# Kernel tuning notes

Measured on AMD Instinct MI355X. Metric: run time of the kernel, lower is better.

## Reference

```python
import jax, jax.numpy as jnp
import numpy as np

N_NODES = 100000
N_EDGES = 1600000
IN_DIM = 128
HID_DIM = 256
OUT_DIM = 128
K = 10
ALPHA = 0.1


def setup_inputs() -> dict:
    key = jax.random.key(0)
    k1, k2, k3, k4, k5, k6, k7 = jax.random.split(key, 7)
    feat = jax.random.normal(k1, (N_NODES, IN_DIM), dtype=jnp.float32)
    src = jax.random.randint(k2, (N_EDGES,), 0, N_NODES, dtype=jnp.int64)
    dst = jax.random.randint(k3, (N_EDGES,), 0, N_NODES, dtype=jnp.int64)
    # MLP params (Linear: y = x @ W + b), kaiming-ish scale
    W1 = jax.random.normal(k4, (IN_DIM, HID_DIM), dtype=jnp.float32) * (1.0 / np.sqrt(IN_DIM))
    b1 = jax.random.normal(k5, (HID_DIM,), dtype=jnp.float32) * 0.01
    W2 = jax.random.normal(k6, (HID_DIM, OUT_DIM), dtype=jnp.float32) * (1.0 / np.sqrt(HID_DIM))
    b2 = jax.random.normal(k7, (OUT_DIM,), dtype=jnp.float32) * 0.01
    return {"feat": feat, "W1": W1, "b1": b1, "W2": W2, "b2": b2, "src": src, "dst": dst}


def reference(feat, W1, b1, W2, b2, src, dst):
    N = feat.shape[0]
    # dgl.add_self_loop: append (i, i) for every node
    loops = jnp.arange(N, dtype=src.dtype)
    src_sl = jnp.concatenate([src, loops])
    dst_sl = jnp.concatenate([dst, loops])
    # symmetric normalization from in-degrees (with self-loops), clamped >= 1
    deg = jax.ops.segment_sum(jnp.ones_like(dst_sl, dtype=feat.dtype), dst_sl, num_segments=N)
    norm = jnp.clip(deg, 1.0) ** -0.5  # [N]

    # APPNP propagation: h <- (1-alpha) * D^-1/2 A D^-1/2 h + alpha * feat
    def hop(h, _):
        m = (h * norm[:, None])[src_sl]                      # gather scaled src feats [E+N, D]
        agg = jax.ops.segment_sum(m, dst_sl, num_segments=N)  # scatter-sum to dst [N, D]
        h = (1.0 - ALPHA) * (agg * norm[:, None]) + ALPHA * feat
        return h, None

    h, _ = jax.lax.scan(hop, feat, None, length=K)
    # 2-layer MLP: Linear -> ReLU -> Linear
    x = jax.nn.relu(h @ W1 + b1)
    return x @ W2 + b2
```

## Files before the change

kernel.cpp:

```cpp
#include <hip/hip_runtime.h>

#define IN_DIM 128
#define HID_DIM 256
#define OUT_DIM 128
#define KHOPS 10

#define NBUCK 32
#define NBLK_B 640

typedef __attribute__((ext_vector_type(8))) short bf16x8;
typedef __attribute__((ext_vector_type(4))) float f32x4;

__device__ __forceinline__ unsigned short f2bf(float x) {
    unsigned int b = __float_as_uint(x);
    unsigned int r = (b + 0x7FFFu + ((b >> 16) & 1u)) >> 16;
    return (unsigned short)r;
}
__device__ __forceinline__ unsigned int pack_bf2(float lo, float hi) {
    return (unsigned int)f2bf(lo) | ((unsigned int)f2bf(hi) << 16);
}
__device__ __forceinline__ float bf_lo(unsigned int u) { return __uint_as_float(u << 16); }
__device__ __forceinline__ float bf_hi(unsigned int u) { return __uint_as_float(u & 0xFFFF0000u); }


__global__ void count_init(int* __restrict__ cnt, int* __restrict__ fill,
                           int* __restrict__ bucket_cnt, int N) {
    int i = blockIdx.x * blockDim.x + threadIdx.x;
    if (i < N) { cnt[i] = 0; fill[i] = 0; }
    if (i < NBUCK) bucket_cnt[i] = 0;
}

__global__ __launch_bounds__(256) void bucket_count(
    const int* __restrict__ dst, int* __restrict__ bucket_cnt,
    int* __restrict__ blk_base, int E) {
    __shared__ int h[NBUCK];
    int tid = threadIdx.x;
    if (tid < NBUCK) h[tid] = 0;
    __syncthreads();
    for (int e = blockIdx.x * 256 + tid; e < E; e += NBLK_B * 256)
        atomicAdd(&h[dst[e] >> 12], 1);
    __syncthreads();
    if (tid < NBUCK)
        blk_base[blockIdx.x * NBUCK + tid] = atomicAdd(&bucket_cnt[tid], h[tid]);
}

__global__ void bucket_scan(const int* __restrict__ bucket_cnt,
                            int* __restrict__ bucket_start) {
    __shared__ int s[NBUCK];
    int tid = threadIdx.x;
    int v = bucket_cnt[tid];
    s[tid] = v;
    __syncthreads();
    for (int off = 1; off < NBUCK; off <<= 1) {
        int t = (tid >= off) ? s[tid - off] : 0;
        __syncthreads();
        s[tid] += t;
        __syncthreads();
    }
    bucket_start[tid] = s[tid] - v;
}

__global__ __launch_bounds__(256) void bucket_fill(
    const int* __restrict__ src, const int* __restrict__ dst,
    const int* __restrict__ bucket_start, const int* __restrict__ blk_base,
    uint2* __restrict__ pairs, int E) {
    __shared__ int base[NBUCK];
    int tid = threadIdx.x;
    if (tid < NBUCK) base[tid] = bucket_start[tid] + blk_base[blockIdx.x * NBUCK + tid];
    __syncthreads();
    for (int e = blockIdx.x * 256 + tid; e < E; e += NBLK_B * 256) {
        int d = dst[e], s = src[e];
        int p = atomicAdd(&base[d >> 12], 1);
        pairs[p] = make_uint2((unsigned)s, (unsigned)d);
    }
}

__global__ void count_pairs(const uint2* __restrict__ pairs, int* __restrict__ cnt, int E) {
    int e = blockIdx.x * blockDim.x + threadIdx.x;
    if (e < E) atomicAdd(&cnt[pairs[e].y], 1);
}

__global__ void norm_kernel(const int* __restrict__ cnt, float* __restrict__ norm, int N) {
    int i = blockIdx.x * blockDim.x + threadIdx.x;
    if (i < N) {
        float deg = (float)(cnt[i] + 1);
        norm[i] = rsqrtf(deg);
    }
}

__global__ void scan_block(const int* __restrict__ cnt, int* __restrict__ row_ptr,
                           int* __restrict__ bsum, int N) {
    __shared__ int s[256];
    int tid = threadIdx.x;
    int gid = blockIdx.x * 256 + tid;
    int v = (gid < N) ? cnt[gid] : 0;
    s[tid] = v;
    __syncthreads();
    for (int off = 1; off < 256; off <<= 1) {
        int t = (tid >= off) ? s[tid - off] : 0;
        __syncthreads();
        s[tid] += t;
        __syncthreads();
    }
    if (gid < N) row_ptr[gid] = s[tid] - v;
    if (tid == 255) bsum[blockIdx.x] = s[255];
}

__global__ void scan_top(int* __restrict__ bsum, int nb) {
    __shared__ int s[512];
    int tid = threadIdx.x;
    int v = (tid < nb) ? bsum[tid] : 0;
    s[tid] = v;
    __syncthreads();
    for (int off = 1; off < 512; off <<= 1) {
        int t = (tid >= off) ? s[tid - off] : 0;
        __syncthreads();
        s[tid] += t;
        __syncthreads();
    }
    if (tid < nb) bsum[tid] = s[tid] - v;
}

__global__ void scan_add(int* __restrict__ row_ptr, const int* __restrict__ bsum,
                         int N, int E) {
    int gid = blockIdx.x * 256 + threadIdx.x;
    if (gid < N) row_ptr[gid] += bsum[blockIdx.x];
    if (gid == 0) row_ptr[N] = E;
}

__global__ void fill_pairs(const uint2* __restrict__ pairs, const int* __restrict__ row_ptr,
                           int* __restrict__ fill, int* __restrict__ col, int E) {
    int e = blockIdx.x * blockDim.x + threadIdx.x;
    if (e < E) {
        uint2 pr = pairs[e];
        int p = atomicAdd(&fill[pr.y], 1);
        col[row_ptr[pr.y] + p] = (int)pr.x;
    }
}


__global__ void pack_w1(const float* __restrict__ W1, short* __restrict__ W1s) {
    int i = blockIdx.x * 256 + threadIdx.x;
    if (i >= 16 * 4 * 64 * 8) return;
    int j = i & 7, l = (i >> 3) & 63, kf = (i >> 9) & 3, rf = i >> 11;
    int k = kf * 32 + (l >> 4) * 8 + j;
    int r = rf * 16 + (l & 15);
    W1s[i] = (short)f2bf(W1[(size_t)k * HID_DIM + r]);
}

__global__ void pack_w2(const float* __restrict__ W2, short* __restrict__ W2s) {
    int i = blockIdx.x * 256 + threadIdx.x;
    if (i >= 8 * 8 * 64 * 8) return;
    int j = i & 7, l = (i >> 3) & 63, kf = (i >> 9) & 7, rf = i >> 12;
    int k = kf * 32 + (l >> 4) * 8 + j;
    int r = rf * 16 + (l & 15);
    W2s[i] = (short)f2bf(W2[(size_t)k * OUT_DIM + r]);
}


__global__ void init_g(const float* __restrict__ feat, const float* __restrict__ norm,
                       unsigned int* __restrict__ sh, unsigned int* __restrict__ ffeat,
                       int N) {
    int idx = blockIdx.x * blockDim.x + threadIdx.x;
    int total = N * 64;
    if (idx >= total) return;
    int row = idx >> 6;
    int l   = idx & 63;
    float nr = norm[row];
    float2 f = *(const float2*)(feat + (size_t)row * IN_DIM + l * 2);
    sh[idx]    = pack_bf2(nr * f.x, nr * f.y);
    ffeat[idx] = pack_bf2(0.1f * nr * f.x, 0.1f * nr * f.y);
}

__global__ __launch_bounds__(256) void hop_kernel(
    const unsigned int* __restrict__ sh_in, unsigned int* __restrict__ sh_out,
    const unsigned int* __restrict__ ffeat, const float* __restrict__ norm,
    const int* __restrict__ row_ptr, const int* __restrict__ col,
    int N) {
    int node = __builtin_amdgcn_readfirstlane(blockIdx.x * 4 + (threadIdx.x >> 6));
    int lane = threadIdx.x & 63;
    if (node >= N) return;
    size_t base = (size_t)node * 64 + lane;
    unsigned int uself = sh_in[base];
    float2 acc = { bf_lo(uself), bf_hi(uself) };
    int beg = row_ptr[node], end = row_ptr[node + 1];
    int e = beg;
    for (; e + 7 < end; e += 8) {
        int s0 = col[e],     s1 = col[e + 1], s2 = col[e + 2], s3 = col[e + 3];
        int s4 = col[e + 4], s5 = col[e + 5], s6 = col[e + 6], s7 = col[e + 7];
        unsigned int u0 = sh_in[(size_t)s0 * 64 + lane];
        unsigned int u1 = sh_in[(size_t)s1 * 64 + lane];
        unsigned int u2 = sh_in[(size_t)s2 * 64 + lane];
        unsigned int u3 = sh_in[(size_t)s3 * 64 + lane];
        unsigned int u4 = sh_in[(size_t)s4 * 64 + lane];
        unsigned int u5 = sh_in[(size_t)s5 * 64 + lane];
        unsigned int u6 = sh_in[(size_t)s6 * 64 + lane];
        unsigned int u7 = sh_in[(size_t)s7 * 64 + lane];
        acc.x += (bf_lo(u0) + bf_lo(u1)) + (bf_lo(u2) + bf_lo(u3))
               + (bf_lo(u4) + bf_lo(u5)) + (bf_lo(u6) + bf_lo(u7));
        acc.y += (bf_hi(u0) + bf_hi(u1)) + (bf_hi(u2) + bf_hi(u3))
               + (bf_hi(u4) + bf_hi(u5)) + (bf_hi(u6) + bf_hi(u7));
    }
    for (; e < end; ++e) {
        unsigned int u = sh_in[(size_t)col[e] * 64 + lane];
        acc.x += bf_lo(u);
        acc.y += bf_hi(u);
    }
    float nr = norm[node];
    float c1 = 0.9f * nr * nr;
    unsigned int uff = ffeat[base];
    float ox = c1 * acc.x + bf_lo(uff);
    float oy = c1 * acc.y + bf_hi(uff);
    sh_out[base] = pack_bf2(ox, oy);
}


#define LDA 136
#define LDH 264

__global__ __launch_bounds__(256) void mlp_mfma(
    const unsigned int* __restrict__ sh, const float* __restrict__ norm,
    const short* __restrict__ W1s, const float* __restrict__ b1,
    const short* __restrict__ W2s, const float* __restrict__ b2,
    float* __restrict__ out, int N)
{
    __shared__ short Ah[64 * LDA];
    __shared__ short Hid[64 * LDH];
    int tid  = threadIdx.x;
    int wid  = tid >> 6;
    int lane = tid & 63;
    int row0 = blockIdx.x * 64;

    for (int i = tid; i < 64 * 64; i += 256) {
        int r = i >> 6, c = i & 63;
        int row = row0 + r;
        unsigned int u = 0;
        float inv = 1.f;
        if (row < N) { u = sh[(size_t)row * 64 + c]; inv = 1.0f / norm[row]; }
        *(unsigned int*)&Ah[r * LDA + c * 2] = pack_bf2(bf_lo(u) * inv, bf_hi(u) * inv);
    }
    __syncthreads();

    int m = lane & 15;
    int g = lane >> 4;

    {
        bf16x8 Bf[4][4];
        #pragma unroll
        for (int kf = 0; kf < 4; ++kf)
            #pragma unroll
            for (int cf = 0; cf < 4; ++cf)
                Bf[kf][cf] = *(const bf16x8*)&Ah[(cf * 16 + m) * LDA + kf * 32 + g * 8];

        f32x4 acc[4][4];
        #pragma unroll
        for (int i = 0; i < 4; ++i)
            #pragma unroll
            for (int cf = 0; cf < 4; ++cf)
                acc[i][cf] = (f32x4){0.f, 0.f, 0.f, 0.f};

        #pragma unroll
        for (int i = 0; i < 4; ++i) {
            int rf = wid * 4 + i;
            #pragma unroll
            for (int kf = 0; kf < 4; ++kf) {
                bf16x8 Af = *(const bf16x8*)(W1s + (((size_t)(rf * 4 + kf)) * 64 + lane) * 8);
                #pragma unroll
                for (int cf = 0; cf < 4; ++cf)
                    acc[i][cf] = __builtin_amdgcn_mfma_f32_16x16x32_bf16(
                        Af, Bf[kf][cf], acc[i][cf], 0, 0, 0);
            }
        }

        #pragma unroll
        for (int i = 0; i < 4; ++i) {
            int feat0 = (wid * 4 + i) * 16 + g * 4;
            float4 bias = *(const float4*)(b1 + feat0);
            #pragma unroll
            for (int cf = 0; cf < 4; ++cf) {
                int node = cf * 16 + m;
                float v0 = acc[i][cf][0] + bias.x; v0 = v0 > 0.f ? v0 : 0.f;
                float v1 = acc[i][cf][1] + bias.y; v1 = v1 > 0.f ? v1 : 0.f;
                float v2 = acc[i][cf][2] + bias.z; v2 = v2 > 0.f ? v2 : 0.f;
                float v3 = acc[i][cf][3] + bias.w; v3 = v3 > 0.f ? v3 : 0.f;
                uint2 p;
                p.x = pack_bf2(v0, v1);
                p.y = pack_bf2(v2, v3);
                *(uint2*)&Hid[node * LDH + feat0] = p;
            }
        }
    }
    __syncthreads();

    {
        f32x4 acc2[2][4];
        #pragma unroll
        for (int i = 0; i < 2; ++i)
            #pragma unroll
            for (int cf = 0; cf < 4; ++cf)
                acc2[i][cf] = (f32x4){0.f, 0.f, 0.f, 0.f};

        #pragma unroll
        for (int kf = 0; kf < 8; ++kf) {
            bf16x8 Bh[4];
            #pragma unroll
            for (int cf = 0; cf < 4; ++cf)
                Bh[cf] = *(const bf16x8*)&Hid[(cf * 16 + m) * LDH + kf * 32 + g * 8];
            #pragma unroll
            for (int i = 0; i < 2; ++i) {
                int rf = wid * 2 + i;
                bf16x8 Af = *(const bf16x8*)(W2s + (((size_t)(rf * 8 + kf)) * 64 + lane) * 8);
                #pragma unroll
                for (int cf = 0; cf < 4; ++cf)
                    acc2[i][cf] = __builtin_amdgcn_mfma_f32_16x16x32_bf16(
                        Af, Bh[cf], acc2[i][cf], 0, 0, 0);
            }
        }

        #pragma unroll
        for (int i = 0; i < 2; ++i) {
            int feat0 = (wid * 2 + i) * 16 + g * 4;
            float4 bias = *(const float4*)(b2 + feat0);
            #pragma unroll
            for (int cf = 0; cf < 4; ++cf) {
                int node = row0 + cf * 16 + m;
                if (node < N) {
                    float4 o;
                    o.x = acc2[i][cf][0] + bias.x;
                    o.y = acc2[i][cf][1] + bias.y;
                    o.z = acc2[i][cf][2] + bias.z;
                    o.w = acc2[i][cf][3] + bias.w;
                    *(float4*)(out + (size_t)node * OUT_DIM + feat0) = o;
                }
            }
        }
    }
}


extern "C" void kernel_launch(void* const* d_in, const int* in_sizes, int n_in,
                              void* d_out, int out_size, void* d_ws, size_t ws_size,
                              hipStream_t stream) {
    const float* feat = (const float*)d_in[0];
    const float* W1   = (const float*)d_in[1];
    const float* b1   = (const float*)d_in[2];
    const float* W2   = (const float*)d_in[3];
    const float* b2   = (const float*)d_in[4];
    const int*   src  = (const int*)d_in[5];
    const int*   dst  = (const int*)d_in[6];
    float* out = (float*)d_out;

    int N = in_sizes[0] / IN_DIM;
    int E = in_sizes[5];

    size_t off = 0;
    auto carve = [&](size_t bytes) -> void* {
        void* p = (char*)d_ws + off;
        off += (bytes + 255) & ~(size_t)255;
        return p;
    };
    float* norm    = (float*)carve((size_t)N * 4);
    int*   cnt     = (int*)carve((size_t)N * 4);
    int*   row_ptr = (int*)carve((size_t)(N + 1) * 4);
    int*   fill    = (int*)carve((size_t)N * 4);
    int*   bsum    = (int*)carve(512 * 4);
    int*   col     = (int*)carve((size_t)E * 4);
    unsigned int* shA   = (unsigned int*)carve((size_t)N * 64 * 4);
    unsigned int* shB   = (unsigned int*)carve((size_t)N * 64 * 4);
    unsigned int* ffeat = (unsigned int*)carve((size_t)N * 64 * 4);
    short* W1s = (short*)carve((size_t)16 * 4 * 64 * 8 * 2);
    short* W2s = (short*)carve((size_t)8 * 8 * 64 * 8 * 2);
    int*   bucket_cnt   = (int*)carve(NBUCK * 4);
    int*   bucket_start = (int*)carve(NBUCK * 4);
    int*   blk_base     = (int*)carve((size_t)NBLK_B * NBUCK * 4);
    uint2* pairs        = (uint2*)carve((size_t)E * 8);
    (void)ws_size;

    int nbN = (N + 255) / 256;
    int nbE = (E + 255) / 256;

    count_init<<<nbN, 256, 0, stream>>>(cnt, fill, bucket_cnt, N);
    bucket_count<<<NBLK_B, 256, 0, stream>>>(dst, bucket_cnt, blk_base, E);
    bucket_scan<<<1, NBUCK, 0, stream>>>(bucket_cnt, bucket_start);
    bucket_fill<<<NBLK_B, 256, 0, stream>>>(src, dst, bucket_start, blk_base, pairs, E);
    count_pairs<<<nbE, 256, 0, stream>>>(pairs, cnt, E);
    norm_kernel<<<nbN, 256, 0, stream>>>(cnt, norm, N);
    scan_block<<<nbN, 256, 0, stream>>>(cnt, row_ptr, bsum, N);
    scan_top<<<1, 512, 0, stream>>>(bsum, nbN);
    scan_add<<<nbN, 256, 0, stream>>>(row_ptr, bsum, N, E);
    fill_pairs<<<nbE, 256, 0, stream>>>(pairs, row_ptr, fill, col, E);

    pack_w1<<<128, 256, 0, stream>>>(W1, W1s);
    pack_w2<<<256, 256, 0, stream>>>(W2, W2s);

    int nbG = ((size_t)N * 64 + 255) / 256;
    init_g<<<nbG, 256, 0, stream>>>(feat, norm, shA, ffeat, N);

    int nbHop = (N + 3) / 4;
    for (int t = 0; t < KHOPS; ++t) {
        const unsigned int* si = (t % 2 == 0) ? shA : shB;
        unsigned int*       so = (t % 2 == 0) ? shB : shA;
        hop_kernel<<<nbHop, 256, 0, stream>>>(si, so, ffeat, norm, row_ptr, col, N);
    }

    int nbM = (N + 63) / 64;
    mlp_mfma<<<nbM, 256, 0, stream>>>(shA, norm, W1s, b1, W2s, b2, out, N);
}
```

Baseline: 859.6 us.

## Build CSR per sub-bucket with LDS histograms and LDS-staged column fill

Degree counting and CSR column fill move from global-atomic per-edge kernels to per-1024-node blocks that scan their bucket's edges and use shared-memory atomics and staging. Edge pairs are packed into 32 bits (source plus low destination bits), which halves the pair buffer. This removes the count/fill zero-init and global atomic contention. In exchange, each bucket is re-read by 4 blocks, only about 98 blocks launch, and the 32-bit packing assumes fewer than 2^17 nodes.

```diff
diff --git a/kernel.cpp b/kernel.cpp
--- a/kernel.cpp
+++ b/kernel.cpp
@@ -7,6 +7,7 @@
 
 #define NBUCK 32
 #define NBLK_B 640
+#define SUBCAP 20480
 
 typedef __attribute__((ext_vector_type(8))) short bf16x8;
 typedef __attribute__((ext_vector_type(4))) float f32x4;
@@ -23,11 +24,8 @@
 __device__ __forceinline__ float bf_hi(unsigned int u) { return __uint_as_float(u & 0xFFFF0000u); }
 
 
-__global__ void count_init(int* __restrict__ cnt, int* __restrict__ fill,
-                           int* __restrict__ bucket_cnt, int N) {
-    int i = blockIdx.x * blockDim.x + threadIdx.x;
-    if (i < N) { cnt[i] = 0; fill[i] = 0; }
-    if (i < NBUCK) bucket_cnt[i] = 0;
+__global__ void zero32(int* __restrict__ bucket_cnt) {
+    if (threadIdx.x < NBUCK) bucket_cnt[threadIdx.x] = 0;
 }
 
 __global__ __launch_bounds__(256) void bucket_count(
@@ -63,7 +61,7 @@
 __global__ __launch_bounds__(256) void bucket_fill(
     const int* __restrict__ src, const int* __restrict__ dst,
     const int* __restrict__ bucket_start, const int* __restrict__ blk_base,
-    uint2* __restrict__ pairs, int E) {
+    unsigned int* __restrict__ pairs, int E) {
     __shared__ int base[NBUCK];
     int tid = threadIdx.x;
     if (tid < NBUCK) base[tid] = bucket_start[tid] + blk_base[blockIdx.x * NBUCK + tid];
@@ -71,13 +69,31 @@
     for (int e = blockIdx.x * 256 + tid; e < E; e += NBLK_B * 256) {
         int d = dst[e], s = src[e];
         int p = atomicAdd(&base[d >> 12], 1);
-        pairs[p] = make_uint2((unsigned)s, (unsigned)d);
-    }
-}
-
-__global__ void count_pairs(const uint2* __restrict__ pairs, int* __restrict__ cnt, int E) {
-    int e = blockIdx.x * blockDim.x + threadIdx.x;
-    if (e < E) atomicAdd(&cnt[pairs[e].y], 1);
+        pairs[p] = (unsigned int)s | ((unsigned int)(d & 4095) << 17);
+    }
+}
+
+__global__ __launch_bounds__(256) void hist_lds(
+    const unsigned int* __restrict__ pairs, const int* __restrict__ bucket_start,
+    int* __restrict__ cnt, int N, int E) {
+    int sb = blockIdx.x;
+    int pb = sb >> 2;
+    int node0 = sb << 10;
+    if (node0 >= N) return;
+    int node1 = min(node0 + 1024, N);
+    int ebeg = bucket_start[pb];
+    int eend = (pb + 1 < NBUCK) ? bucket_start[pb + 1] : E;
+    int sub = sb & 3;
+    __shared__ int h[1024];
+    for (int i = threadIdx.x; i < 1024; i += 256) h[i] = 0;
+    __syncthreads();
+    for (int e = ebeg + threadIdx.x; e < eend; e += 256) {
+        unsigned int p = pairs[e];
+        int dlow = p >> 17;
+        if ((dlow >> 10) == sub) atomicAdd(&h[dlow & 1023], 1);
+    }
+    __syncthreads();
+    for (int i = threadIdx.x; i < node1 - node0; i += 256) cnt[node0 + i] = h[i];
 }
 
 __global__ void norm_kernel(const int* __restrict__ cnt, float* __restrict__ norm, int N) {
@@ -128,14 +144,37 @@
     if (gid == 0) row_ptr[N] = E;
 }
 
-__global__ void fill_pairs(const uint2* __restrict__ pairs, const int* __restrict__ row_ptr,
-                           int* __restrict__ fill, int* __restrict__ col, int E) {
-    int e = blockIdx.x * blockDim.x + threadIdx.x;
-    if (e < E) {
-        uint2 pr = pairs[e];
-        int p = atomicAdd(&fill[pr.y], 1);
-        col[row_ptr[pr.y] + p] = (int)pr.x;
-    }
+__global__ __launch_bounds__(256) void fill_lds(
+    const unsigned int* __restrict__ pairs, const int* __restrict__ bucket_start,
+    const int* __restrict__ row_ptr, int* __restrict__ col, int N, int E) {
+    int sb = blockIdx.x;
+    int pb = sb >> 2;
+    int node0 = sb << 10;
+    if (node0 >= N) return;
+    int node1 = min(node0 + 1024, N);
+    int ebeg = bucket_start[pb];
+    int eend = (pb + 1 < NBUCK) ? bucket_start[pb + 1] : E;
+    int sub = sb & 3;
+    int base_col = row_ptr[node0];
+    int seg = row_ptr[node1] - base_col;
+    __shared__ int lfill[1024];
+    __shared__ int lcol[SUBCAP];
+    for (int i = threadIdx.x; i < 1024; i += 256) lfill[i] = 0;
+    __syncthreads();
+    for (int e = ebeg + threadIdx.x; e < eend; e += 256) {
+        unsigned int p = pairs[e];
+        int dlow = p >> 17;
+        if ((dlow >> 10) != sub) continue;
+        int d = (pb << 12) | dlow;
+        int s = (int)(p & 0x1FFFFu);
+        int idx = atomicAdd(&lfill[dlow & 1023], 1);
+        int pos = row_ptr[d] - base_col + idx;
+        if (pos < SUBCAP) lcol[pos] = s;
+        else col[base_col + pos] = s;
+    }
+    __syncthreads();
+    int n_out = seg < SUBCAP ? seg : SUBCAP;
+    for (int i = threadIdx.x; i < n_out; i += 256) col[base_col + i] = lcol[i];
 }
 
 
@@ -362,7 +401,6 @@
     float* norm    = (float*)carve((size_t)N * 4);
     int*   cnt     = (int*)carve((size_t)N * 4);
     int*   row_ptr = (int*)carve((size_t)(N + 1) * 4);
-    int*   fill    = (int*)carve((size_t)N * 4);
     int*   bsum    = (int*)carve(512 * 4);
     int*   col     = (int*)carve((size_t)E * 4);
     unsigned int* shA   = (unsigned int*)carve((size_t)N * 64 * 4);
@@ -373,22 +411,22 @@
     int*   bucket_cnt   = (int*)carve(NBUCK * 4);
     int*   bucket_start = (int*)carve(NBUCK * 4);
     int*   blk_base     = (int*)carve((size_t)NBLK_B * NBUCK * 4);
-    uint2* pairs        = (uint2*)carve((size_t)E * 8);
+    unsigned int* pairs = (unsigned int*)carve((size_t)E * 4);
     (void)ws_size;
 
     int nbN = (N + 255) / 256;
-    int nbE = (E + 255) / 256;
-
-    count_init<<<nbN, 256, 0, stream>>>(cnt, fill, bucket_cnt, N);
+    int nbSB = (N + 1023) / 1024;
+
+    zero32<<<1, 32, 0, stream>>>(bucket_cnt);
     bucket_count<<<NBLK_B, 256, 0, stream>>>(dst, bucket_cnt, blk_base, E);
     bucket_scan<<<1, NBUCK, 0, stream>>>(bucket_cnt, bucket_start);
     bucket_fill<<<NBLK_B, 256, 0, stream>>>(src, dst, bucket_start, blk_base, pairs, E);
-    count_pairs<<<nbE, 256, 0, stream>>>(pairs, cnt, E);
+    hist_lds<<<nbSB, 256, 0, stream>>>(pairs, bucket_start, cnt, N, E);
     norm_kernel<<<nbN, 256, 0, stream>>>(cnt, norm, N);
     scan_block<<<nbN, 256, 0, stream>>>(cnt, row_ptr, bsum, N);
     scan_top<<<1, 512, 0, stream>>>(bsum, nbN);
     scan_add<<<nbN, 256, 0, stream>>>(row_ptr, bsum, N, E);
-    fill_pairs<<<nbE, 256, 0, stream>>>(pairs, row_ptr, fill, col, E);
+    fill_lds<<<nbSB, 256, 0, stream>>>(pairs, bucket_start, row_ptr, col, N, E);
 
     pack_w1<<<128, 256, 0, stream>>>(W1, W1s);
     pack_w2<<<256, 256, 0, stream>>>(W2, W2s);
```

New measurement: 908.9 us. 1.06x slower.
